# Performance work log

Measured on AMD Instinct MI355X. Metric: run time of the kernel, lower is better.

## Reference

```python
import jax, jax.numpy as jnp
import numpy as np

B, S, E, H = 2, 2048, 1024, 16
D = E // H  # head_dim = 64
SCALE = D ** -0.5
NEG = -1e9


def setup_inputs() -> dict:
    key = jax.random.key(0)
    ks = jax.random.split(key, 10)
    hidden_states = jax.random.normal(ks[0], (B, S, E), dtype=jnp.float32)
    # CLIP-style additive causal mask [B, 1, L, S]
    causal = jnp.where(jnp.tril(jnp.ones((S, S), dtype=bool)), 0.0, NEG).astype(jnp.float32)
    attn_mask = jnp.broadcast_to(causal, (B, 1, S, S))
    def lin(kw, kb):
        W = jax.random.normal(kw, (E, E), dtype=jnp.float32) * (E ** -0.5)
        b = jax.random.normal(kb, (E,), dtype=jnp.float32) * 0.02
        return W, b
    Wq, bq = lin(ks[1], ks[2])
    Wk, bk = lin(ks[3], ks[4])
    Wv, bv = lin(ks[5], ks[6])
    Wo, bo = lin(ks[7], ks[8])
    return {"hidden_states": hidden_states, "attn_mask": attn_mask,
            "Wq": Wq, "bq": bq, "Wk": Wk, "bk": bk,
            "Wv": Wv, "bv": bv, "Wo": Wo, "bo": bo}


def reference(hidden_states, attn_mask, Wq, bq, Wk, bk, Wv, bv, Wo, bo):
    b, L, e = hidden_states.shape
    # projections (nn.Linear: x @ W.T + b)
    def split_heads(x):
        return x.reshape(b, L, H, D).transpose(0, 2, 1, 3)  # [b,h,l,d]
    q = split_heads(hidden_states @ Wq.T + bq)
    k = split_heads(hidden_states @ Wk.T + bk)
    v = split_heads(hidden_states @ Wv.T + bv)
    # QK^T * scale + additive mask, softmax, AV (dropout_p = 0 in eval)
    scores = jnp.einsum('bhld,bhsd->bhls', q, k) * SCALE + attn_mask
    attn = jax.nn.softmax(scores, axis=-1)
    ctx = jnp.einsum('bhls,bhsd->bhld', attn, v)
    ctx = ctx.transpose(0, 2, 1, 3).reshape(b, L, e)
    return ctx @ Wo.T + bo
```

## Files before the change

### kernel.cpp

```cpp
#include <hip/hip_runtime.h>
#include <hip/hip_bf16.h>
#include <stdint.h>


typedef __hip_bfloat16 bf16;
typedef short bf16x8 __attribute__((ext_vector_type(8)));
typedef short bf16x4 __attribute__((ext_vector_type(4)));
typedef float f32x4 __attribute__((ext_vector_type(4)));

__device__ __forceinline__ f32x4 mfma16(bf16x8 a, bf16x8 b, f32x4 c) {
  return __builtin_amdgcn_mfma_f32_16x16x32_bf16(a, b, c, 0, 0, 0);
}

__device__ __forceinline__ f32x4 mfma_k16(bf16x4 a, bf16x4 b, f32x4 c) {
#if __has_builtin(__builtin_amdgcn_mfma_f32_16x16x16bf16_1k)
  return __builtin_amdgcn_mfma_f32_16x16x16bf16_1k(a, b, c, 0, 0, 0);
#else
  f32x4 d;
  asm volatile("v_mfma_f32_16x16x16_bf16 %0, %1, %2, %3\n\ts_nop 7\n\ts_nop 7"
               : "=v"(d)
               : "v"(a), "v"(b), "v"(c));
  return d;
#endif
}

__device__ __forceinline__ void async16(const void* g, void* l) {
  __builtin_amdgcn_global_load_lds((const __attribute__((address_space(1))) void*)g,
                                   (__attribute__((address_space(3))) void*)l, 16, 0, 0);
}

__global__ __launch_bounds__(256) void cvt_kernel(
    const float* __restrict__ hs, const float* __restrict__ Wq,
    const float* __restrict__ Wk, const float* __restrict__ Wv,
    const float* __restrict__ Wo, bf16* __restrict__ dst) {
  const size_t e = ((size_t)blockIdx.x * 256 + threadIdx.x) * 8;
  const float* src;
  size_t off;
  if (e < 4194304) {
    src = hs; off = e;
  } else {
    const size_t w = e - 4194304;
    const int wi = (int)(w >> 20);
    src = (wi == 0) ? Wq : (wi == 1) ? Wk : (wi == 2) ? Wv : Wo;
    off = w & 1048575;
  }
  const float4 a = *(const float4*)(src + off);
  const float4 b = *(const float4*)(src + off + 4);
  union { bf16 h[8]; uint4 u; } p;
  p.h[0] = __float2bfloat16(a.x); p.h[1] = __float2bfloat16(a.y);
  p.h[2] = __float2bfloat16(a.z); p.h[3] = __float2bfloat16(a.w);
  p.h[4] = __float2bfloat16(b.x); p.h[5] = __float2bfloat16(b.y);
  p.h[6] = __float2bfloat16(b.z); p.h[7] = __float2bfloat16(b.w);
  *(uint4*)(dst + e) = p.u;
}

__global__ __launch_bounds__(256, 3) void qkv_gemm(
    const bf16* __restrict__ X, const bf16* __restrict__ Wb,
    const float* __restrict__ bq, const float* __restrict__ bk,
    const float* __restrict__ bv, bf16* __restrict__ out) {
  constexpr int Kd = 1024;
  __shared__ bf16 sA[2][128 * 32];
  __shared__ bf16 sB[2][128 * 32];
  const int tid = threadIdx.x;
  const int wave = tid >> 6, lane = tid & 63;
  const int g = lane >> 4, ln = lane & 15;
  const int tM = blockIdx.y * 128, tN = blockIdx.x * 128;
  const int which = tN >> 10;
  const bf16* W = Wb + (size_t)which * 1048576;
  const float* bias = (which == 0) ? bq : (which == 1) ? bk : bv;
  const int tNl = tN & 1023;
  const float oscale = (which == 0) ? 0.18033688011112042f : 1.0f;
  const int wrow = (wave >> 1) * 64, wcol = (wave & 1) * 64;
  const f32x4 fz = {0.f, 0.f, 0.f, 0.f};

  f32x4 acc[4][4];
#pragma unroll
  for (int i = 0; i < 4; ++i)
#pragma unroll
    for (int j = 0; j < 4; ++j) acc[i][j] = fz;

  int srow[4], scol[4];
#pragma unroll
  for (int t = 0; t < 4; ++t) {
    const int d = tid + t * 256;
    srow[t] = (d >> 2) & 127;
    scol[t] = ((d >> 9) << 5) + ((d & 3) << 3);
  }

  for (int k0 = 0; k0 < Kd; k0 += 64) {
    __syncthreads();
#pragma unroll
    for (int t = 0; t < 4; ++t) {
      const int d = tid + t * 256;
      async16(X + (size_t)(tM + srow[t]) * Kd + k0 + scol[t], &sA[0][0] + d * 8);
      async16(W + (size_t)(tNl + srow[t]) * Kd + k0 + scol[t], &sB[0][0] + d * 8);
    }
    __syncthreads();
#pragma unroll
    for (int kk = 0; kk < 2; ++kk) {
      bf16x8 aF[4], bF[4];
#pragma unroll
      for (int i = 0; i < 4; ++i)
        aF[i] = *(const bf16x8*)(&sA[kk][0] + (wrow + i * 16 + ln) * 32 + g * 8);
#pragma unroll
      for (int j = 0; j < 4; ++j)
        bF[j] = *(const bf16x8*)(&sB[kk][0] + (wcol + j * 16 + ln) * 32 + g * 8);
#pragma unroll
      for (int i = 0; i < 4; ++i)
#pragma unroll
        for (int j = 0; j < 4; ++j) acc[i][j] = mfma16(aF[i], bF[j], acc[i][j]);
    }
  }

  bf16* outw = out + (size_t)which * 4194304;
  if (which == 2) {
#pragma unroll
    for (int j = 0; j < 4; ++j) {
      const int nl = tNl + wcol + j * 16 + ln;
      const float bvf = bias[nl];
      const int h = nl >> 6, d = nl & 63;
#pragma unroll
      for (int i = 0; i < 4; ++i) {
        const int m0 = tM + wrow + i * 16 + g * 4;
        const int b = m0 >> 11, s0 = m0 & 2047;
        union { bf16 hh[4]; bf16x4 v; } pk;
#pragma unroll
        for (int r = 0; r < 4; ++r) pk.hh[r] = __float2bfloat16(acc[i][j][r] + bvf);
        *(bf16x4*)(outw + (((size_t)(b * 16 + h) * 64 + d) << 11) + s0) = pk.v;
      }
    }
  } else {
#pragma unroll
    for (int j = 0; j < 4; ++j) {
      const int nl = tNl + wcol + j * 16 + ln;
      const float bvf = bias[nl];
      const int h = nl >> 6, d = nl & 63;
#pragma unroll
      for (int i = 0; i < 4; ++i) {
#pragma unroll
        for (int r = 0; r < 4; ++r) {
          const int m = tM + wrow + i * 16 + g * 4 + r;
          const int b = m >> 11, s = m & 2047;
          const float v = (acc[i][j][r] + bvf) * oscale;
          outw[(((size_t)(b * 16 + h) * 2048 + s) << 6) + d] = __float2bfloat16(v);
        }
      }
    }
  }
}

__global__ __launch_bounds__(256, 4) void out_gemm(
    const bf16* __restrict__ X, const bf16* __restrict__ W,
    const float* __restrict__ bias, float* __restrict__ out) {
  constexpr int Kd = 1024;
  __shared__ bf16 sA[64 * 32];
  __shared__ bf16 sB[64 * 32];
  const int tid = threadIdx.x;
  const int wave = tid >> 6, lane = tid & 63;
  const int g = lane >> 4, ln = lane & 15;
  const int tM = blockIdx.y * 64, tN = blockIdx.x * 64;
  const f32x4 fz = {0.f, 0.f, 0.f, 0.f};

  f32x4 acc[4];
#pragma unroll
  for (int j = 0; j < 4; ++j) acc[j] = fz;

  const int srow = tid >> 2, scol = (tid & 3) << 3;
  for (int k0 = 0; k0 < Kd; k0 += 32) {
    __syncthreads();
    async16(X + (size_t)(tM + srow) * Kd + k0 + scol, sA + tid * 8);
    async16(W + (size_t)(tN + srow) * Kd + k0 + scol, sB + tid * 8);
    __syncthreads();
    const bf16x8 aF = *(const bf16x8*)(sA + (wave * 16 + ln) * 32 + g * 8);
    bf16x8 bF[4];
#pragma unroll
    for (int j = 0; j < 4; ++j)
      bF[j] = *(const bf16x8*)(sB + (j * 16 + ln) * 32 + g * 8);
#pragma unroll
    for (int j = 0; j < 4; ++j) acc[j] = mfma16(aF, bF[j], acc[j]);
  }

#pragma unroll
  for (int j = 0; j < 4; ++j) {
    const int n = tN + j * 16 + ln;
    const float bvf = bias[n];
#pragma unroll
    for (int r = 0; r < 4; ++r) {
      const int m = tM + wave * 16 + g * 4 + r;
      out[(size_t)m * 1024 + n] = acc[j][r] + bvf;
    }
  }
}

__global__ __launch_bounds__(256, 4) void attn_kernel(
    const bf16* __restrict__ Q, const bf16* __restrict__ K,
    const bf16* __restrict__ V, bf16* __restrict__ O) {
  constexpr int S = 2048, D = 64;
  __shared__ bf16 sK[64 * 72];
  __shared__ bf16 sVt[2][64 * 64];

  const int tid = threadIdx.x;
  const int w = tid >> 6, lane = tid & 63;
  const int g = lane >> 4, ln = lane & 15;
  const int px = blockIdx.x, py = blockIdx.y;
  const int bh = (px & 7) * 4 + (py & 3);
  const int s = py >> 3;
  const int q0 = (px >> 3) + 4 * ((py >> 2) & 1);
  const int qt = (s == 0) ? 31 - q0
               : (s == 1) ? 16 + q0
               : (s == 2) ? 15 - q0
                          : q0;
  const int b = bh >> 4, h = bh & 15;
  const f32x4 fz = {0.f, 0.f, 0.f, 0.f};

  const bf16* Qb = Q + (size_t)bh * S * D;
  const bf16* Kb = K + (size_t)bh * S * D;
  const bf16* Vt = V + (size_t)bh * 64 * 2048;

  const int kr0 = tid >> 3, kc0 = (tid & 7) << 3;
  int voff[2];
#pragma unroll
  for (int t = 0; t < 2; ++t) {
    const int p = tid + t * 256;
    const int d = p >> 3, cc = p & 7;
    voff[t] = d * 2048 + ((cc ^ ((d & 3) << 1)) << 3);
  }

  bf16x8 qf[2];
#pragma unroll
  for (int kc = 0; kc < 2; ++kc)
    qf[kc] = *(const bf16x8*)(Qb + (size_t)(qt * 64 + w * 16 + ln) * D + kc * 32 + g * 8);

  f32x4 oacc[4];
#pragma unroll
  for (int db = 0; db < 4; ++db) oacc[db] = fz;
  f32x4 lacc = fz;
  const short onebf = (short)0x3F80;
  const bf16x4 onesf = {onebf, onebf, onebf, onebf};

  int sx[4];
  {
    const int s8b = g >> 1, xr = (ln & 3) << 1, vlo = (g & 1) << 2;
#pragma unroll
    for (int kb = 0; kb < 4; ++kb) sx[kb] = (((2 * kb + s8b) ^ xr) << 3) + vlo;
  }

  uint4 kreg0 = *(const uint4*)(Kb + (size_t)kr0 * D + kc0);
  uint4 kreg1 = *(const uint4*)(Kb + (size_t)(kr0 + 32) * D + kc0);
  async16(Vt + voff[0], &sVt[0][0] + tid * 8);
  async16(Vt + voff[1], &sVt[0][0] + (tid + 256) * 8);

  for (int kt = 0; kt <= qt; ++kt) {
    __syncthreads();
    *(uint4*)(sK + kr0 * 72 + kc0) = kreg0;
    *(uint4*)(sK + (kr0 + 32) * 72 + kc0) = kreg1;
    __syncthreads();
    if (kt < qt) {
      const int nb = (kt + 1) << 6;
      bf16* vb = &sVt[(kt + 1) & 1][0];
      async16(Vt + voff[0] + nb, vb + tid * 8);
      async16(Vt + voff[1] + nb, vb + (tid + 256) * 8);
      const size_t nr = (size_t)nb;
      kreg0 = *(const uint4*)(Kb + (nr + kr0) * D + kc0);
      kreg1 = *(const uint4*)(Kb + (nr + kr0 + 32) * D + kc0);
    }

    f32x4 sacc[4];
#pragma unroll
    for (int kb = 0; kb < 4; ++kb) sacc[kb] = fz;
#pragma unroll
    for (int kb = 0; kb < 4; ++kb) {
      const bf16x8 k0 = *(const bf16x8*)(sK + (kb * 16 + ln) * 72 + g * 8);
      const bf16x8 k1 = *(const bf16x8*)(sK + (kb * 16 + ln) * 72 + 32 + g * 8);
      sacc[kb] = mfma16(k0, qf[0], sacc[kb]);
      sacc[kb] = mfma16(k1, qf[1], sacc[kb]);
    }

    const bool diag = (kt == qt);
    const int qloc = w * 16 + ln;
    bf16x4 pa[4];
#pragma unroll
    for (int kb = 0; kb < 4; ++kb) {
      union { bf16 hh[4]; bf16x4 v; } pu;
#pragma unroll
      for (int r = 0; r < 4; ++r) {
        float pv = exp2f(sacc[kb][r]);
        if (diag && (kb * 16 + g * 4 + r > qloc)) pv = 0.f;
        pu.hh[r] = __float2bfloat16(pv);
      }
      pa[kb] = pu.v;
      lacc = mfma_k16(pa[kb], onesf, lacc);
    }

    const bf16* sVc = &sVt[kt & 1][0];
#pragma unroll
    for (int db = 0; db < 4; ++db) {
      const int rowb = (db * 16 + ln) * 64;
#pragma unroll
      for (int kb = 0; kb < 4; ++kb) {
        const bf16x4 vf = *(const bf16x4*)(sVc + rowb + sx[kb]);
        oacc[db] = mfma_k16(pa[kb], vf, oacc[db]);
      }
    }
  }

  float invl[4];
#pragma unroll
  for (int r = 0; r < 4; ++r) invl[r] = 1.0f / lacc[r];

#pragma unroll
  for (int db = 0; db < 4; ++db)
#pragma unroll
    for (int r = 0; r < 4; ++r) {
      const int row = qt * 64 + w * 16 + g * 4 + r;
      const int col = db * 16 + ln;
      O[(((size_t)(b * 2048 + row) * 16 + h) << 6) + col] =
          __float2bfloat16(oacc[db][r] * invl[r]);
    }
}

extern "C" void kernel_launch(void* const* d_in, const int* in_sizes, int n_in,
                              void* d_out, int out_size, void* d_ws, size_t ws_size,
                              hipStream_t stream) {
  const float* hs = (const float*)d_in[0];
  const float* Wq = (const float*)d_in[2];
  const float* bq = (const float*)d_in[3];
  const float* Wk = (const float*)d_in[4];
  const float* bk = (const float*)d_in[5];
  const float* Wv = (const float*)d_in[6];
  const float* bv = (const float*)d_in[7];
  const float* Wo = (const float*)d_in[8];
  const float* bo = (const float*)d_in[9];
  float* out = (float*)d_out;

  char* ws = (char*)d_ws;
  bf16* XW = (bf16*)ws;
  bf16* Xb = XW;
  bf16* W3b = XW + 4194304;
  bf16* Wob = XW + 7340032;
  bf16* Qw = (bf16*)(ws + (16u << 20));
  bf16* Kw = (bf16*)(ws + (24u << 20));
  bf16* Vw = (bf16*)(ws + (32u << 20));
  bf16* Cw = (bf16*)ws;

  const dim3 blk(256);
  cvt_kernel<<<4096, blk, 0, stream>>>(hs, Wq, Wk, Wv, Wo, XW);
  qkv_gemm<<<dim3(24, 32), blk, 0, stream>>>(Xb, W3b, bq, bk, bv, Qw);
  attn_kernel<<<dim3(32, 32), blk, 0, stream>>>(Qw, Kw, Vw, Cw);
  out_gemm<<<dim3(16, 64), blk, 0, stream>>>(Cw, Wob, bo, out);
}
```

Measured before the change: 209.3 us.

## Store V in MFMA fragment order so attention copies tiles contiguously

The QKV projection epilogue now writes V in a per-(batch, head, 64-key tile) layout that matches the MFMA B-operand fragment order, rather than transposed [d][s]. The attention kernel then copies each 4096-element V tile into shared memory with contiguous 16-byte async loads and reads fragments with linear, conflict-free addressing. This removes the XOR swizzle and the strided global V loads. The cost is that the producer's global stores are scattered in a new pattern, and both kernels now depend on this private layout.

```diff
diff --git a/kernel.cpp b/kernel.cpp
--- a/kernel.cpp
+++ b/kernel.cpp
@@ -114,19 +114,20 @@
 
   bf16* outw = out + (size_t)which * 4194304;
   if (which == 2) {
+    const int hh = (tNl + wcol) >> 6;
 #pragma unroll
     for (int j = 0; j < 4; ++j) {
       const int nl = tNl + wcol + j * 16 + ln;
       const float bvf = bias[nl];
-      const int h = nl >> 6, d = nl & 63;
 #pragma unroll
       for (int i = 0; i < 4; ++i) {
         const int m0 = tM + wrow + i * 16 + g * 4;
-        const int b = m0 >> 11, s0 = m0 & 2047;
-        union { bf16 hh[4]; bf16x4 v; } pk;
-#pragma unroll
-        for (int r = 0; r < 4; ++r) pk.hh[r] = __float2bfloat16(acc[i][j][r] + bvf);
-        *(bf16x4*)(outw + (((size_t)(b * 16 + h) * 64 + d) << 11) + s0) = pk.v;
+        const int b = m0 >> 11, t = (m0 & 2047) >> 6;
+        union { bf16 hv[4]; bf16x4 v; } pk;
+#pragma unroll
+        for (int r = 0; r < 4; ++r) pk.hv[r] = __float2bfloat16(acc[i][j][r] + bvf);
+        *(bf16x4*)(outw + (((size_t)(b * 16 + hh) * 32 + t) << 12) +
+                   (i * 4 + j) * 256 + (g * 16 + ln) * 4) = pk.v;
       }
     }
   } else {
@@ -197,7 +198,7 @@
     const bf16* __restrict__ V, bf16* __restrict__ O) {
   constexpr int S = 2048, D = 64;
   __shared__ bf16 sK[64 * 72];
-  __shared__ bf16 sVt[2][64 * 64];
+  __shared__ bf16 sVf[2][64 * 64];
 
   const int tid = threadIdx.x;
   const int w = tid >> 6, lane = tid & 63;
@@ -215,16 +216,9 @@
 
   const bf16* Qb = Q + (size_t)bh * S * D;
   const bf16* Kb = K + (size_t)bh * S * D;
-  const bf16* Vt = V + (size_t)bh * 64 * 2048;
+  const bf16* Vfb = V + (size_t)bh * 131072;
 
   const int kr0 = tid >> 3, kc0 = (tid & 7) << 3;
-  int voff[2];
-#pragma unroll
-  for (int t = 0; t < 2; ++t) {
-    const int p = tid + t * 256;
-    const int d = p >> 3, cc = p & 7;
-    voff[t] = d * 2048 + ((cc ^ ((d & 3) << 1)) << 3);
-  }
 
   bf16x8 qf[2];
 #pragma unroll
@@ -238,17 +232,10 @@
   const short onebf = (short)0x3F80;
   const bf16x4 onesf = {onebf, onebf, onebf, onebf};
 
-  int sx[4];
-  {
-    const int s8b = g >> 1, xr = (ln & 3) << 1, vlo = (g & 1) << 2;
-#pragma unroll
-    for (int kb = 0; kb < 4; ++kb) sx[kb] = (((2 * kb + s8b) ^ xr) << 3) + vlo;
-  }
-
   uint4 kreg0 = *(const uint4*)(Kb + (size_t)kr0 * D + kc0);
   uint4 kreg1 = *(const uint4*)(Kb + (size_t)(kr0 + 32) * D + kc0);
-  async16(Vt + voff[0], &sVt[0][0] + tid * 8);
-  async16(Vt + voff[1], &sVt[0][0] + (tid + 256) * 8);
+  async16(Vfb + tid * 8, &sVf[0][0] + tid * 8);
+  async16(Vfb + 2048 + tid * 8, &sVf[0][0] + 2048 + tid * 8);
 
   for (int kt = 0; kt <= qt; ++kt) {
     __syncthreads();
@@ -256,13 +243,13 @@
     *(uint4*)(sK + (kr0 + 32) * 72 + kc0) = kreg1;
     __syncthreads();
     if (kt < qt) {
-      const int nb = (kt + 1) << 6;
-      bf16* vb = &sVt[(kt + 1) & 1][0];
-      async16(Vt + voff[0] + nb, vb + tid * 8);
-      async16(Vt + voff[1] + nb, vb + (tid + 256) * 8);
-      const size_t nr = (size_t)nb;
-      kreg0 = *(const uint4*)(Kb + (nr + kr0) * D + kc0);
-      kreg1 = *(const uint4*)(Kb + (nr + kr0 + 32) * D + kc0);
+      const bf16* vs = Vfb + (kt + 1) * 4096;
+      bf16* vb = &sVf[(kt + 1) & 1][0];
+      async16(vs + tid * 8, vb + tid * 8);
+      async16(vs + 2048 + tid * 8, vb + 2048 + tid * 8);
+      const size_t nb = (size_t)(kt + 1) * 64;
+      kreg0 = *(const uint4*)(Kb + (nb + kr0) * D + kc0);
+      kreg1 = *(const uint4*)(Kb + (nb + kr0 + 32) * D + kc0);
     }
 
     f32x4 sacc[4];
@@ -292,13 +279,13 @@
       lacc = mfma_k16(pa[kb], onesf, lacc);
     }
 
-    const bf16* sVc = &sVt[kt & 1][0];
+    const bf16* sVc = &sVf[kt & 1][0];
 #pragma unroll
     for (int db = 0; db < 4; ++db) {
-      const int rowb = (db * 16 + ln) * 64;
 #pragma unroll
       for (int kb = 0; kb < 4; ++kb) {
-        const bf16x4 vf = *(const bf16x4*)(sVc + rowb + sx[kb]);
+        const bf16x4 vf =
+            *(const bf16x4*)(sVc + ((kb * 4 + db) * 64 + g * 16 + ln) * 4);
         oacc[db] = mfma_k16(pa[kb], vf, oacc[db]);
       }
     }
```

Result: faster. 194.8 us (-6.9%).
